# Kernel tuning notes

Measured on AMD Instinct MI355X. Metric: run time of the kernel, lower is better.

## Reference

```python
import jax, jax.numpy as jnp
import numpy as np

ROPE_BASE = 10000.0

def _rope_cos_sin(T, d, dtype):
    inv_freq = 1.0 / (ROPE_BASE ** (jnp.arange(0, d, 2, dtype=jnp.float32) / d))
    t = jnp.arange(T, dtype=jnp.float32)
    freqs = t[:, None] * inv_freq[None, :]           # [T, d/2]
    emb = jnp.concatenate([freqs, freqs], axis=-1)   # [T, d]
    return jnp.cos(emb).astype(dtype), jnp.sin(emb).astype(dtype)

def _rotate_half(x):
    x1, x2 = jnp.split(x, 2, axis=-1)
    return jnp.concatenate([-x2, x1], axis=-1)

def setup_inputs() -> dict:
    key = jax.random.key(0)
    k1, k2, k3, k4 = jax.random.split(key, 4)
    B, T, C, H = 4, 4096, 1024, 64
    x = jax.random.normal(k1, (B, T, C), dtype=jnp.float32)
    s = 1.0 / np.sqrt(C)
    Wq = jax.random.normal(k2, (H, C), dtype=jnp.float32) * s
    Wk = jax.random.normal(k3, (H, C), dtype=jnp.float32) * s
    Wv = jax.random.normal(k4, (H, C), dtype=jnp.float32) * s
    return {"x": x, "Wq": Wq, "Wk": Wk, "Wv": Wv}

def reference(x, Wq, Wk, Wv):
    B, T, C = x.shape
    H = Wq.shape[0]
    q = jnp.einsum('btc,hc->bth', x, Wq)
    k = jnp.einsum('btc,hc->bth', x, Wk)
    v = jnp.einsum('btc,hc->bth', x, Wv)
    cos, sin = _rope_cos_sin(T, H, x.dtype)
    q = q * cos + _rotate_half(q) * sin
    k = k * cos + _rotate_half(k) * sin
    # NOTE: original scales by dim_model**-0.5 (C), not head_size
    wei = jnp.einsum('bth,bsh->bts', q, k) * (C ** -0.5)
    causal = jnp.tril(jnp.ones((T, T), dtype=bool))
    wei = jnp.where(causal, wei, -jnp.inf)
    wei = jax.nn.softmax(wei, axis=-1)
    # dropout p=0.0 (identity)
    out = jnp.einsum('bts,bsh->bth', wei, v)
    return out
```

## Files before the change

kernel.cpp:

```cpp
#include <hip/hip_runtime.h>
#include <hip/hip_bf16.h>
#include <math.h>

typedef __attribute__((ext_vector_type(8))) __bf16 bf16x8;
typedef __attribute__((ext_vector_type(4))) float f32x4;
typedef __attribute__((ext_vector_type(16))) float f32x16;
typedef __attribute__((ext_vector_type(4))) float float4_t;
typedef __attribute__((ext_vector_type(4))) unsigned int uint4_t;

#define NB 4
#define TSEQ 4096
#define CD 1024
#define HD 64
#define NCH 8
#define CHT 8
#define QBL 16

static __device__ __forceinline__ unsigned short f2bf(float f) {
    union { float f; unsigned u; } v; v.f = f;
    unsigned r = v.u + 0x7fffu + ((v.u >> 16) & 1u);
    return (unsigned short)(r >> 16);
}
static __device__ __forceinline__ float bf2f(unsigned short u) {
    union { unsigned int i; float f; } v; v.i = ((unsigned int)u) << 16;
    return v.f;
}
static __device__ __forceinline__ unsigned int pk2(float a, float b) {
    union { __bf16 h[2]; unsigned int u; } x;
    x.h[0] = (__bf16)a; x.h[1] = (__bf16)b;
    return x.u;
}

__global__ __launch_bounds__(256) void wcvt_kernel(const float* __restrict__ wq,
                                                   const float* __restrict__ wk,
                                                   const float* __restrict__ wv,
                                                   unsigned short* __restrict__ wb) {
    int i = blockIdx.x * 256 + threadIdx.x;
    int j = i >> 10;
    int col = i & 1023;
    int jb = j >> 4, off = j & 15;
    int sub = ((jb & 1) << 5) | ((jb & 2) << 3);
    int srcrow = (jb < 8) ? (sub + off) : ((jb - 8) * 16 + off);
    const float* src = (jb < 4) ? wq : ((jb < 8) ? wk : wv);
    wb[i] = f2bf(src[srcrow * 1024 + col]);
}

__global__ __launch_bounds__(256) void qkv_kernel(const float* __restrict__ x,
                                                  const unsigned short* __restrict__ wb,
                                                  unsigned short* __restrict__ qo,
                                                  unsigned short* __restrict__ ko,
                                                  unsigned short* __restrict__ vt) {
    __shared__ unsigned short xs[64][72];
    __shared__ unsigned short ws[64][72];
    const int tid = threadIdx.x;
    const int wave = tid >> 6, lane = tid & 63;
    const int lr = lane & 15;
    const int lk = (lane >> 4) << 3;
    const int rowg = (lane >> 4) << 2;
    const int row0 = blockIdx.x * 64;
    const int cbi = blockIdx.y;
    const int cb = cbi * 64;

    f32x4 acc[4];
#pragma unroll
    for (int i = 0; i < 4; ++i) acc[i] = (f32x4){0.f, 0.f, 0.f, 0.f};

    const int sr = tid >> 2;
    const int sc = (tid & 3) << 4;

    float4_t xf0, xf1, xf2, xf3;
    uint4_t wf0, wf1;
    auto loadregs = [&](int k0) {
        const float4_t* s4 =
            reinterpret_cast<const float4_t*>(x + (size_t)(row0 + sr) * CD + k0 + sc);
        xf0 = s4[0]; xf1 = s4[1]; xf2 = s4[2]; xf3 = s4[3];
        const uint4_t* wsrc =
            reinterpret_cast<const uint4_t*>(wb + (size_t)(cb + sr) * CD + k0 + sc);
        wf0 = wsrc[0]; wf1 = wsrc[1];
    };

    loadregs(0);

    for (int k0 = 0; k0 < CD; k0 += 64) {
        __syncthreads();
        {
            uint4_t w0, w1;
            w0[0] = pk2(xf0[0], xf0[1]); w0[1] = pk2(xf0[2], xf0[3]);
            w0[2] = pk2(xf1[0], xf1[1]); w0[3] = pk2(xf1[2], xf1[3]);
            w1[0] = pk2(xf2[0], xf2[1]); w1[1] = pk2(xf2[2], xf2[3]);
            w1[2] = pk2(xf3[0], xf3[1]); w1[3] = pk2(xf3[2], xf3[3]);
            *reinterpret_cast<uint4_t*>(&xs[sr][sc]) = w0;
            *reinterpret_cast<uint4_t*>(&xs[sr][sc + 8]) = w1;
            *reinterpret_cast<uint4_t*>(&ws[sr][sc]) = wf0;
            *reinterpret_cast<uint4_t*>(&ws[sr][sc + 8]) = wf1;
        }
        __syncthreads();
        if (k0 + 64 < CD) loadregs(k0 + 64);
#pragma unroll
        for (int kk = 0; kk < 2; ++kk) {
            bf16x8 a = *reinterpret_cast<const bf16x8*>(&xs[wave * 16 + lr][kk * 32 + lk]);
#pragma unroll
            for (int c = 0; c < 4; ++c) {
                bf16x8 bfr = *reinterpret_cast<const bf16x8*>(&ws[c * 16 + lr][kk * 32 + lk]);
                acc[c] = __builtin_amdgcn_mfma_f32_16x16x32_bf16(a, bfr, acc[c], 0, 0, 0);
            }
        }
    }

    const int gr0 = row0 + wave * 16 + rowg;
    const int bidx = gr0 >> 12;
    const int tb = gr0 & (TSEQ - 1);
    if (cbi < 2) {
        unsigned short* o = (cbi == 0) ? qo : ko;
        const float sc2 = (cbi == 0) ? 0.045084218764560315f : 1.0f;
        const float l2b = 0.4152410118609215f;
        const float invf0 = exp2f(-(float)lr * l2b);
        const float invf1 = exp2f(-(float)(lr + 16) * l2b);
#pragma unroll
        for (int r = 0; r < 4; ++r) {
            float t = (float)(tb + r);
            float s0, c0, s1, c1;
            sincosf(t * invf0, &s0, &c0);
            sincosf(t * invf1, &s1, &c1);
            size_t ro = (size_t)(gr0 + r) * HD;
            float lo, hi;
            lo = acc[0][r]; hi = acc[1][r];
            o[ro + 0 + lr]  = f2bf((lo * c0 - hi * s0) * sc2);
            o[ro + 32 + lr] = f2bf((hi * c0 + lo * s0) * sc2);
            lo = acc[2][r]; hi = acc[3][r];
            o[ro + 16 + lr] = f2bf((lo * c1 - hi * s1) * sc2);
            o[ro + 48 + lr] = f2bf((hi * c1 + lo * s1) * sc2);
        }
    } else {
#pragma unroll
        for (int r = 0; r < 4; ++r) {
            size_t vbase = (size_t)bidx * HD * TSEQ + (size_t)(tb + r);
            vt[vbase + (size_t)(0 + lr) * TSEQ]  = f2bf(acc[0][r]);
            vt[vbase + (size_t)(16 + lr) * TSEQ] = f2bf(acc[1][r]);
            vt[vbase + (size_t)(32 + lr) * TSEQ] = f2bf(acc[2][r]);
            vt[vbase + (size_t)(48 + lr) * TSEQ] = f2bf(acc[3][r]);
        }
    }
}

__global__ __launch_bounds__(512, 4) void attn_partial(const unsigned short* __restrict__ q,
                                                       const unsigned short* __restrict__ k,
                                                       const unsigned short* __restrict__ vt,
                                                       unsigned short* __restrict__ po,
                                                       float* __restrict__ pm,
                                                       float* __restrict__ pl) {
    const int chunk = blockIdx.x, qb = blockIdx.y, b = blockIdx.z;
    const int ktend_blk = 4 * qb + 3;
    const int kt0 = chunk * CHT;
    if (kt0 > ktend_blk) return;
    const int ktend = min(ktend_blk, kt0 + CHT - 1);
    const int nt = ktend - kt0 + 1;

    __shared__ unsigned short ks[2][64][72];
    __shared__ unsigned short vs[2][64][72];
    const int tid = threadIdx.x;
    const int wave = tid >> 6, lane = tid & 63;
    const int l31 = lane & 31;
    const int h = lane >> 5;
    const int h8 = h << 3;
    const int qrow0 = qb * 256 + wave * 32;
    const int qpos = qrow0 + l31;

    const unsigned short* qb_ = q + ((size_t)(b * TSEQ + qpos)) * HD + h8;
    bf16x8 qf[4];
#pragma unroll
    for (int s = 0; s < 4; ++s)
        qf[s] = *reinterpret_cast<const bf16x8*>(qb_ + 16 * s);

    f32x16 oacc[2];
#pragma unroll
    for (int dt = 0; dt < 2; ++dt)
#pragma unroll
        for (int r = 0; r < 16; ++r) oacc[dt][r] = 0.f;
    float mreg = -1.0e30f;
    float lsum = 0.f;

    const int srow = tid >> 3;
    const int scol = (tid & 7) << 3;
    const unsigned short* kbase = k + (size_t)b * TSEQ * HD;
    const unsigned short* vbase = vt + (size_t)b * HD * TSEQ;
    uint4_t kr, vr;

    auto loadtile = [&](int kt) {
        const int s0l = kt * 64;
        kr = *reinterpret_cast<const uint4_t*>(kbase + (size_t)(s0l + srow) * HD + scol);
        vr = *reinterpret_cast<const uint4_t*>(vbase + (size_t)srow * TSEQ + s0l + scol);
    };
    auto writetile = [&](int p) {
        *reinterpret_cast<uint4_t*>(&ks[p][srow][scol]) = kr;
        *reinterpret_cast<uint4_t*>(&vs[p][srow][scol]) = vr;
    };

    loadtile(kt0);
    writetile(0);
    if (nt > 1) loadtile(kt0 + 1);
    __syncthreads();

    for (int it = 0; it < nt; ++it) {
        const int kt = kt0 + it;
        const int s0 = kt * 64;
        const int p = it & 1;
        if (it + 1 < nt) {
            writetile(p ^ 1);
            if (it + 2 < nt) loadtile(kt + 2);
        }

        if (s0 <= qrow0 + 31) {
            f32x16 sacc[2];
#pragma unroll
            for (int blk = 0; blk < 2; ++blk)
#pragma unroll
                for (int r = 0; r < 16; ++r) sacc[blk][r] = 0.f;
            __builtin_amdgcn_s_setprio(1);
#pragma unroll
            for (int s = 0; s < 4; ++s) {
                bf16x8 ka = *reinterpret_cast<const bf16x8*>(&ks[p][l31][16 * s + h8]);
                bf16x8 kb2 = *reinterpret_cast<const bf16x8*>(&ks[p][32 + l31][16 * s + h8]);
                sacc[0] = __builtin_amdgcn_mfma_f32_32x32x16_bf16(ka, qf[s], sacc[0], 0, 0, 0);
                sacc[1] = __builtin_amdgcn_mfma_f32_32x32x16_bf16(kb2, qf[s], sacc[1], 0, 0, 0);
            }
            __builtin_amdgcn_s_setprio(0);

            if (s0 + 63 > qrow0) {
#pragma unroll
                for (int blk = 0; blk < 2; ++blk)
#pragma unroll
                    for (int r = 0; r < 16; ++r) {
                        int kvpos = s0 + 32 * blk + (r & 3) + ((r >> 2) << 3) + (h << 2);
                        if (kvpos > qpos) sacc[blk][r] = -INFINITY;
                    }
            }

            float tm[8];
#pragma unroll
            for (int r = 0; r < 8; ++r)
                tm[r] = fmaxf(fmaxf(sacc[0][r], sacc[0][r + 8]),
                              fmaxf(sacc[1][r], sacc[1][r + 8]));
#pragma unroll
            for (int r = 0; r < 4; ++r) tm[r] = fmaxf(tm[r], tm[r + 4]);
            float mx = fmaxf(fmaxf(tm[0], tm[1]), fmaxf(tm[2], tm[3]));
            mx = fmaxf(mx, __shfl_xor(mx, 32, 64));

            const bool newmax = !__all(mx <= mreg + 7.0f);
            if (newmax) {
                float mnew = fmaxf(mreg, mx);
                float corr = __builtin_amdgcn_exp2f(mreg - mnew);
                mreg = mnew;
                lsum *= corr;
#pragma unroll
                for (int dt = 0; dt < 2; ++dt)
#pragma unroll
                    for (int r = 0; r < 16; ++r) oacc[dt][r] *= corr;
            }

            float pvv[2][16];
#pragma unroll
            for (int blk = 0; blk < 2; ++blk)
#pragma unroll
                for (int r = 0; r < 16; ++r)
                    pvv[blk][r] = __builtin_amdgcn_exp2f(sacc[blk][r] - mreg);
            float ts[8];
#pragma unroll
            for (int r = 0; r < 8; ++r)
                ts[r] = (pvv[0][r] + pvv[0][r + 8]) + (pvv[1][r] + pvv[1][r + 8]);
#pragma unroll
            for (int r = 0; r < 4; ++r) ts[r] += ts[r + 4];
            float psum = (ts[0] + ts[1]) + (ts[2] + ts[3]);
            psum += __shfl_xor(psum, 32, 64);
            lsum += psum;

            unsigned int cw[2][4][2];
#pragma unroll
            for (int blk = 0; blk < 2; ++blk)
#pragma unroll
                for (int G = 0; G < 4; ++G) {
                    cw[blk][G][0] = pk2(pvv[blk][4 * G], pvv[blk][4 * G + 1]);
                    cw[blk][G][1] = pk2(pvv[blk][4 * G + 2], pvv[blk][4 * G + 3]);
                }

            const bool hif = (h == 1);
            __builtin_amdgcn_s_setprio(1);
#pragma unroll
            for (int s = 0; s < 4; ++s) {
                const int blk = s >> 1, base = (s & 1) << 1;
                unsigned int a0 = cw[blk][base][0],     a1 = cw[blk][base][1];
                unsigned int b0 = cw[blk][base + 1][0], b1 = cw[blk][base + 1][1];
                unsigned int s0w = hif ? a0 : b0;
                unsigned int s1w = hif ? a1 : b1;
                unsigned int r0 = __shfl_xor(s0w, 32, 64);
                unsigned int r1 = __shfl_xor(s1w, 32, 64);
                uint4_t pw;
                pw[0] = hif ? r0 : a0;
                pw[1] = hif ? r1 : a1;
                pw[2] = hif ? b0 : r0;
                pw[3] = hif ? b1 : r1;
                bf16x8 pfrag = *reinterpret_cast<const bf16x8*>(&pw);
                bf16x8 v0 = *reinterpret_cast<const bf16x8*>(&vs[p][l31][16 * s + h8]);
                bf16x8 v1 = *reinterpret_cast<const bf16x8*>(&vs[p][32 + l31][16 * s + h8]);
                oacc[0] = __builtin_amdgcn_mfma_f32_32x32x16_bf16(v0, pfrag, oacc[0], 0, 0, 0);
                oacc[1] = __builtin_amdgcn_mfma_f32_32x32x16_bf16(v1, pfrag, oacc[1], 0, 0, 0);
            }
            __builtin_amdgcn_s_setprio(0);
        }
        __syncthreads();
    }

    const int slot = (((b << 4) + qb) << 3) + chunk;
    unsigned short* pob = po + (size_t)slot * 16384;
#pragma unroll
    for (int dt = 0; dt < 2; ++dt)
#pragma unroll
        for (int r = 0; r < 16; ++r) {
            int d = 32 * dt + (r & 3) + ((r >> 2) << 3) + (h << 2);
            pob[d * 256 + wave * 32 + l31] = f2bf(oacc[dt][r]);
        }
    if (h == 0) {
        pm[slot * 256 + wave * 32 + l31] = mreg;
        pl[slot * 256 + wave * 32 + l31] = lsum;
    }
}

__global__ __launch_bounds__(256) void attn_combine(const unsigned short* __restrict__ po,
                                                    const float* __restrict__ pm,
                                                    const float* __restrict__ pl,
                                                    float* __restrict__ out) {
    __shared__ float sm[64][17];
    const int bq = blockIdx.x;
    const int dg = blockIdx.y;
    const int qt = bq & 63;
    const int b = bq >> 6;
    const int qb = qt >> 2, quarter = qt & 3;
    const int nch = (4 * qb + 11) >> 3;
    const int qi = threadIdx.x & 63;
    const int jj = threadIdx.x >> 6;
    const int slotb = (((b << 4) + qb) << 3);
    const int qoff = quarter * 64 + qi;

    float pmv[NCH];
#pragma unroll
    for (int c = 0; c < NCH; ++c)
        pmv[c] = (c < nch) ? pm[(size_t)(slotb + c) * 256 + qoff] : -1.0e30f;
    float tmv[NCH];
#pragma unroll
    for (int c = 0; c < NCH; ++c) tmv[c] = pmv[c];
#pragma unroll
    for (int s = NCH / 2; s >= 1; s >>= 1)
#pragma unroll
        for (int c = 0; c < NCH / 2; ++c)
            if (c < s) tmv[c] = fmaxf(tmv[c], tmv[c + s]);
    const float M = tmv[0];

    float L = 0.f;
    float a0 = 0.f, a1 = 0.f, a2 = 0.f, a3 = 0.f;
    const int dbase = dg * 16 + jj * 4;
#pragma unroll 4
    for (int c = 0; c < nch; ++c) {
        float w = exp2f(pmv[c] - M);
        L += w * pl[(size_t)(slotb + c) * 256 + qoff];
        const unsigned short* p = po + (size_t)(slotb + c) * 16384 + dbase * 256 + qoff;
        a0 += w * bf2f(p[0]);
        a1 += w * bf2f(p[256]);
        a2 += w * bf2f(p[512]);
        a3 += w * bf2f(p[768]);
    }
    const float inv = 1.f / L;
    sm[qi][jj * 4 + 0] = a0 * inv;
    sm[qi][jj * 4 + 1] = a1 * inv;
    sm[qi][jj * 4 + 2] = a2 * inv;
    sm[qi][jj * 4 + 3] = a3 * inv;
    __syncthreads();
    const int row = threadIdx.x >> 2;
    const int c4 = (threadIdx.x & 3) << 2;
    float4_t f;
#pragma unroll
    for (int e = 0; e < 4; ++e) f[e] = sm[row][c4 + e];
    *reinterpret_cast<float4_t*>(out + (size_t)bq * 4096 + row * 64 + dg * 16 + c4) = f;
}

extern "C" void kernel_launch(void* const* d_in, const int* in_sizes, int n_in,
                              void* d_out, int out_size, void* d_ws, size_t ws_size,
                              hipStream_t stream) {
    const float* x = (const float*)d_in[0];
    const float* wq = (const float*)d_in[1];
    const float* wk = (const float*)d_in[2];
    const float* wv = (const float*)d_in[3];
    float* out = (float*)d_out;

    unsigned short* wb = (unsigned short*)d_ws;
    unsigned short* qb = wb + 3 * HD * CD;
    unsigned short* kb = qb + (size_t)NB * TSEQ * HD;
    unsigned short* vtb = kb + (size_t)NB * TSEQ * HD;
    unsigned short* pob = vtb + (size_t)NB * TSEQ * HD;
    float* pm = (float*)(pob + (size_t)512 * 16384);
    float* pl = pm + (size_t)512 * 256;

    wcvt_kernel<<<768, 256, 0, stream>>>(wq, wk, wv, wb);
    qkv_kernel<<<dim3(256, 3), 256, 0, stream>>>(x, wb, qb, kb, vtb);
    attn_partial<<<dim3(NCH, QBL, NB), 512, 0, stream>>>(qb, kb, vtb, pob, pm, pl);
    attn_combine<<<dim3(NB * 64, 4), 256, 0, stream>>>(pob, pm, pl, out);
}
```

Measured before the change: 61.37 us.

## Load K/V fragments directly from global memory instead of LDS double buffering

Removes the shared-memory double-buffered K/V staging and the per-tile block barrier. Each wave now loads its K and V MFMA fragments directly from global memory, and the loop breaks early once the tile passes the causal limit. The launch-bounds occupancy hint drops from 4 to 2 blocks per CU to allow more registers. Trading shared-memory traffic and syncs for redundant global/L2 loads across the 8 waves risks higher memory traffic and exposed load latency, since there is no prefetch.

Result: slower. 97.53 us (+58.9%).

```diff
diff --git a/kernel.cpp b/kernel.cpp
--- a/kernel.cpp
+++ b/kernel.cpp
@@ -143,7 +143,7 @@
     }
 }
 
-__global__ __launch_bounds__(512, 4) void attn_partial(const unsigned short* __restrict__ q,
+__global__ __launch_bounds__(512, 2) void attn_partial(const unsigned short* __restrict__ q,
                                                        const unsigned short* __restrict__ k,
                                                        const unsigned short* __restrict__ vt,
                                                        unsigned short* __restrict__ po,
@@ -154,10 +154,7 @@
     const int kt0 = chunk * CHT;
     if (kt0 > ktend_blk) return;
     const int ktend = min(ktend_blk, kt0 + CHT - 1);
-    const int nt = ktend - kt0 + 1;
-
-    __shared__ unsigned short ks[2][64][72];
-    __shared__ unsigned short vs[2][64][72];
+
     const int tid = threadIdx.x;
     const int wave = tid >> 6, lane = tid & 63;
     const int l31 = lane & 31;
@@ -180,134 +177,116 @@
     float mreg = -1.0e30f;
     float lsum = 0.f;
 
-    const int srow = tid >> 3;
-    const int scol = (tid & 7) << 3;
-    const unsigned short* kbase = k + (size_t)b * TSEQ * HD;
-    const unsigned short* vbase = vt + (size_t)b * HD * TSEQ;
-    uint4_t kr, vr;
-
-    auto loadtile = [&](int kt) {
-        const int s0l = kt * 64;
-        kr = *reinterpret_cast<const uint4_t*>(kbase + (size_t)(s0l + srow) * HD + scol);
-        vr = *reinterpret_cast<const uint4_t*>(vbase + (size_t)srow * TSEQ + s0l + scol);
-    };
-    auto writetile = [&](int p) {
-        *reinterpret_cast<uint4_t*>(&ks[p][srow][scol]) = kr;
-        *reinterpret_cast<uint4_t*>(&vs[p][srow][scol]) = vr;
-    };
-
-    loadtile(kt0);
-    writetile(0);
-    if (nt > 1) loadtile(kt0 + 1);
-    __syncthreads();
-
-    for (int it = 0; it < nt; ++it) {
-        const int kt = kt0 + it;
+    const unsigned short* kp0 = k + (size_t)b * TSEQ * HD + (size_t)l31 * HD + h8;
+    const unsigned short* kp1 = kp0 + (size_t)32 * HD;
+    const unsigned short* vp0 = vt + (size_t)b * HD * TSEQ + (size_t)l31 * TSEQ + h8;
+    const unsigned short* vp1 = vp0 + (size_t)32 * TSEQ;
+
+    for (int kt = kt0; kt <= ktend; ++kt) {
         const int s0 = kt * 64;
-        const int p = it & 1;
-        if (it + 1 < nt) {
-            writetile(p ^ 1);
-            if (it + 2 < nt) loadtile(kt + 2);
-        }
-
-        if (s0 <= qrow0 + 31) {
-            f32x16 sacc[2];
+        if (s0 > qrow0 + 31) break;
+
+        bf16x8 kf0[4], kf1[4], vf0[4], vf1[4];
+#pragma unroll
+        for (int s = 0; s < 4; ++s) {
+            const size_t ko_ = (size_t)s0 * HD + 16 * s;
+            kf0[s] = *reinterpret_cast<const bf16x8*>(kp0 + ko_);
+            kf1[s] = *reinterpret_cast<const bf16x8*>(kp1 + ko_);
+            vf0[s] = *reinterpret_cast<const bf16x8*>(vp0 + s0 + 16 * s);
+            vf1[s] = *reinterpret_cast<const bf16x8*>(vp1 + s0 + 16 * s);
+        }
+
+        f32x16 sacc[2];
+#pragma unroll
+        for (int blk = 0; blk < 2; ++blk)
+#pragma unroll
+            for (int r = 0; r < 16; ++r) sacc[blk][r] = 0.f;
+        __builtin_amdgcn_s_setprio(1);
+#pragma unroll
+        for (int s = 0; s < 4; ++s) {
+            sacc[0] = __builtin_amdgcn_mfma_f32_32x32x16_bf16(kf0[s], qf[s], sacc[0], 0, 0, 0);
+            sacc[1] = __builtin_amdgcn_mfma_f32_32x32x16_bf16(kf1[s], qf[s], sacc[1], 0, 0, 0);
+        }
+        __builtin_amdgcn_s_setprio(0);
+
+        if (s0 + 63 > qrow0) {
 #pragma unroll
             for (int blk = 0; blk < 2; ++blk)
 #pragma unroll
-                for (int r = 0; r < 16; ++r) sacc[blk][r] = 0.f;
-            __builtin_amdgcn_s_setprio(1);
-#pragma unroll
-            for (int s = 0; s < 4; ++s) {
-                bf16x8 ka = *reinterpret_cast<const bf16x8*>(&ks[p][l31][16 * s + h8]);
-                bf16x8 kb2 = *reinterpret_cast<const bf16x8*>(&ks[p][32 + l31][16 * s + h8]);
-                sacc[0] = __builtin_amdgcn_mfma_f32_32x32x16_bf16(ka, qf[s], sacc[0], 0, 0, 0);
-                sacc[1] = __builtin_amdgcn_mfma_f32_32x32x16_bf16(kb2, qf[s], sacc[1], 0, 0, 0);
+                for (int r = 0; r < 16; ++r) {
+                    int kvpos = s0 + 32 * blk + (r & 3) + ((r >> 2) << 3) + (h << 2);
+                    if (kvpos > qpos) sacc[blk][r] = -INFINITY;
+                }
+        }
+
+        float tm[8];
+#pragma unroll
+        for (int r = 0; r < 8; ++r)
+            tm[r] = fmaxf(fmaxf(sacc[0][r], sacc[0][r + 8]),
+                          fmaxf(sacc[1][r], sacc[1][r + 8]));
+#pragma unroll
+        for (int r = 0; r < 4; ++r) tm[r] = fmaxf(tm[r], tm[r + 4]);
+        float mx = fmaxf(fmaxf(tm[0], tm[1]), fmaxf(tm[2], tm[3]));
+        mx = fmaxf(mx, __shfl_xor(mx, 32, 64));
+
+        const bool newmax = !__all(mx <= mreg + 7.0f);
+        if (newmax) {
+            float mnew = fmaxf(mreg, mx);
+            float corr = __builtin_amdgcn_exp2f(mreg - mnew);
+            mreg = mnew;
+            lsum *= corr;
+#pragma unroll
+            for (int dt = 0; dt < 2; ++dt)
+#pragma unroll
+                for (int r = 0; r < 16; ++r) oacc[dt][r] *= corr;
+        }
+
+        float pvv[2][16];
+#pragma unroll
+        for (int blk = 0; blk < 2; ++blk)
+#pragma unroll
+            for (int r = 0; r < 16; ++r)
+                pvv[blk][r] = __builtin_amdgcn_exp2f(sacc[blk][r] - mreg);
+        float ts[8];
+#pragma unroll
+        for (int r = 0; r < 8; ++r)
+            ts[r] = (pvv[0][r] + pvv[0][r + 8]) + (pvv[1][r] + pvv[1][r + 8]);
+#pragma unroll
+        for (int r = 0; r < 4; ++r) ts[r] += ts[r + 4];
+        float psum = (ts[0] + ts[1]) + (ts[2] + ts[3]);
+        psum += __shfl_xor(psum, 32, 64);
+        lsum += psum;
+
+        unsigned int cw[2][4][2];
+#pragma unroll
+        for (int blk = 0; blk < 2; ++blk)
+#pragma unroll
+            for (int G = 0; G < 4; ++G) {
+                cw[blk][G][0] = pk2(pvv[blk][4 * G], pvv[blk][4 * G + 1]);
+                cw[blk][G][1] = pk2(pvv[blk][4 * G + 2], pvv[blk][4 * G + 3]);
             }
-            __builtin_amdgcn_s_setprio(0);
-
-            if (s0 + 63 > qrow0) {
-#pragma unroll
-                for (int blk = 0; blk < 2; ++blk)
-#pragma unroll
-                    for (int r = 0; r < 16; ++r) {
-                        int kvpos = s0 + 32 * blk + (r & 3) + ((r >> 2) << 3) + (h << 2);
-                        if (kvpos > qpos) sacc[blk][r] = -INFINITY;
-                    }
-            }
-
-            float tm[8];
-#pragma unroll
-            for (int r = 0; r < 8; ++r)
-                tm[r] = fmaxf(fmaxf(sacc[0][r], sacc[0][r + 8]),
-                              fmaxf(sacc[1][r], sacc[1][r + 8]));
-#pragma unroll
-            for (int r = 0; r < 4; ++r) tm[r] = fmaxf(tm[r], tm[r + 4]);
-            float mx = fmaxf(fmaxf(tm[0], tm[1]), fmaxf(tm[2], tm[3]));
-            mx = fmaxf(mx, __shfl_xor(mx, 32, 64));
-
-            const bool newmax = !__all(mx <= mreg + 7.0f);
-            if (newmax) {
-                float mnew = fmaxf(mreg, mx);
-                float corr = __builtin_amdgcn_exp2f(mreg - mnew);
-                mreg = mnew;
-                lsum *= corr;
-#pragma unroll
-                for (int dt = 0; dt < 2; ++dt)
-#pragma unroll
-                    for (int r = 0; r < 16; ++r) oacc[dt][r] *= corr;
-            }
-
-            float pvv[2][16];
-#pragma unroll
-            for (int blk = 0; blk < 2; ++blk)
-#pragma unroll
-                for (int r = 0; r < 16; ++r)
-                    pvv[blk][r] = __builtin_amdgcn_exp2f(sacc[blk][r] - mreg);
-            float ts[8];
-#pragma unroll
-            for (int r = 0; r < 8; ++r)
-                ts[r] = (pvv[0][r] + pvv[0][r + 8]) + (pvv[1][r] + pvv[1][r + 8]);
-#pragma unroll
-            for (int r = 0; r < 4; ++r) ts[r] += ts[r + 4];
-            float psum = (ts[0] + ts[1]) + (ts[2] + ts[3]);
-            psum += __shfl_xor(psum, 32, 64);
-            lsum += psum;
-
-            unsigned int cw[2][4][2];
-#pragma unroll
-            for (int blk = 0; blk < 2; ++blk)
-#pragma unroll
-                for (int G = 0; G < 4; ++G) {
-                    cw[blk][G][0] = pk2(pvv[blk][4 * G], pvv[blk][4 * G + 1]);
-                    cw[blk][G][1] = pk2(pvv[blk][4 * G + 2], pvv[blk][4 * G + 3]);
-                }
-
-            const bool hif = (h == 1);
-            __builtin_amdgcn_s_setprio(1);
-#pragma unroll
-            for (int s = 0; s < 4; ++s) {
-                const int blk = s >> 1, base = (s & 1) << 1;
-                unsigned int a0 = cw[blk][base][0],     a1 = cw[blk][base][1];
-                unsigned int b0 = cw[blk][base + 1][0], b1 = cw[blk][base + 1][1];
-                unsigned int s0w = hif ? a0 : b0;
-                unsigned int s1w = hif ? a1 : b1;
-                unsigned int r0 = __shfl_xor(s0w, 32, 64);
-                unsigned int r1 = __shfl_xor(s1w, 32, 64);
-                uint4_t pw;
-                pw[0] = hif ? r0 : a0;
-                pw[1] = hif ? r1 : a1;
-                pw[2] = hif ? b0 : r0;
-                pw[3] = hif ? b1 : r1;
-                bf16x8 pfrag = *reinterpret_cast<const bf16x8*>(&pw);
-                bf16x8 v0 = *reinterpret_cast<const bf16x8*>(&vs[p][l31][16 * s + h8]);
-                bf16x8 v1 = *reinterpret_cast<const bf16x8*>(&vs[p][32 + l31][16 * s + h8]);
-                oacc[0] = __builtin_amdgcn_mfma_f32_32x32x16_bf16(v0, pfrag, oacc[0], 0, 0, 0);
-                oacc[1] = __builtin_amdgcn_mfma_f32_32x32x16_bf16(v1, pfrag, oacc[1], 0, 0, 0);
-            }
-            __builtin_amdgcn_s_setprio(0);
-        }
-        __syncthreads();
+
+        const bool hif = (h == 1);
+        __builtin_amdgcn_s_setprio(1);
+#pragma unroll
+        for (int s = 0; s < 4; ++s) {
+            const int blk = s >> 1, base = (s & 1) << 1;
+            unsigned int a0 = cw[blk][base][0],     a1 = cw[blk][base][1];
+            unsigned int b0 = cw[blk][base + 1][0], b1 = cw[blk][base + 1][1];
+            unsigned int s0w = hif ? a0 : b0;
+            unsigned int s1w = hif ? a1 : b1;
+            unsigned int r0 = __shfl_xor(s0w, 32, 64);
+            unsigned int r1 = __shfl_xor(s1w, 32, 64);
+            uint4_t pw;
+            pw[0] = hif ? r0 : a0;
+            pw[1] = hif ? r1 : a1;
+            pw[2] = hif ? b0 : r0;
+            pw[3] = hif ? b1 : r1;
+            bf16x8 pfrag = *reinterpret_cast<const bf16x8*>(&pw);
+            oacc[0] = __builtin_amdgcn_mfma_f32_32x32x16_bf16(vf0[s], pfrag, oacc[0], 0, 0, 0);
+            oacc[1] = __builtin_amdgcn_mfma_f32_32x32x16_bf16(vf1[s], pfrag, oacc[1], 0, 0, 0);
+        }
+        __builtin_amdgcn_s_setprio(0);
     }
 
     const int slot = (((b << 4) + qb) << 3) + chunk;
```
